# Performance work log

Hardware: AMD Instinct MI355X
Metric: run time of the kernel (lower is better)

The kernel has to match this reference:

```python
import jax, jax.numpy as jnp
import numpy as np

N, E, F_IN, HID, HEADS, C, NCLS, NG, NCONV = 50000, 800000, 128, 128, 8, 16, 10, 64, 3
EPS = 1e-5
NEG_SLOPE = 0.2


def bn_eval(x, p):
    # p: [4, dim] = (gamma, beta, running_mean, running_var); eval-mode BatchNorm1d
    g, b, m, v = p[0], p[1], p[2], p[3]
    return g * (x - m) * jax.lax.rsqrt(v + EPS) + b


def gat_conv(x, src, dst, W, a_src, a_dst, bias):
    # PyG GATConv, concat=True, add_self_loops=True, eval (no dropout)
    h = (x @ W).reshape(N, HEADS, C)                    # [N,H,C]
    alpha_s = jnp.sum(h * a_src[None], axis=-1)         # [N,H]
    alpha_d = jnp.sum(h * a_dst[None], axis=-1)         # [N,H]
    loop = jnp.arange(N)
    s = jnp.concatenate([src, loop])                    # [E+N]
    d = jnp.concatenate([dst, loop])
    logits = jax.nn.leaky_relu(alpha_s[s] + alpha_d[d], NEG_SLOPE)   # [E+N,H]
    mx = jax.lax.stop_gradient(jax.ops.segment_max(logits, d, num_segments=N))
    ex = jnp.exp(logits - mx[d])
    denom = jax.ops.segment_sum(ex, d, num_segments=N)
    alpha = ex / (denom[d] + 1e-16)                     # segment softmax over dst
    msg = h[s] * alpha[:, :, None]                      # [E+N,H,C]
    out = jax.ops.segment_sum(msg, d, num_segments=N)   # [N,H,C]
    return out.reshape(N, HEADS * C) + bias


def setup_inputs() -> dict:
    key = jax.random.key(0)
    ks = jax.random.split(key, 16)

    def bn_p(dim):
        return jnp.stack([jnp.ones(dim), jnp.full((dim,), 1e-4), jnp.zeros(dim), jnp.ones(dim)])

    sc = 0.05
    inp = {
        "x": jax.random.normal(ks[0], (N, F_IN), jnp.float32),
        "edge_index": jax.random.randint(ks[1], (2, E), 0, N),
        "batch": jnp.sort(jax.random.randint(ks[2], (N,), 0, NG)),
        "bn_feat_params": bn_p(F_IN),
        "w_feat": jax.random.normal(ks[3], (F_IN, HID), jnp.float32) * sc,
        "b_feat": jnp.zeros((HID,), jnp.float32),
        "bns_conv_params": jnp.stack([bn_p(HID)] * NCONV),
        "gat_w": jax.random.normal(ks[4], (NCONV, HID, HID), jnp.float32) * sc,
        "gat_att_src": jax.random.normal(ks[5], (NCONV, HEADS, C), jnp.float32) * sc,
        "gat_att_dst": jax.random.normal(ks[6], (NCONV, HEADS, C), jnp.float32) * sc,
        "gat_b": jnp.zeros((NCONV, HID), jnp.float32),
        "bns_fc_params": jnp.stack([bn_p(HID)] * 1),
        "fc_w": jax.random.normal(ks[7], (1, HID, HID), jnp.float32) * sc,
        "fc_b": jnp.zeros((1, HID), jnp.float32),
        "bn_hidden_params": bn_p(HID),
        "w_class": jax.random.normal(ks[8], (HID, NCLS), jnp.float32) * sc,
        "b_class": jnp.zeros((NCLS,), jnp.float32),
    }
    return inp


def reference(x, edge_index, batch, bn_feat_params, w_feat, b_feat, bns_conv_params,
              gat_w, gat_att_src, gat_att_dst, gat_b, bns_fc_params, fc_w, fc_b,
              bn_hidden_params, w_class, b_class):
    src, dst = edge_index[0], edge_index[1]
    h = bn_eval(x, bn_feat_params)
    h = jax.nn.relu(h @ w_feat + b_feat)             # GCNConv(gfn=True) == linear
    for i in range(NCONV):
        h = bn_eval(h, bns_conv_params[i])
        h = jax.nn.relu(gat_conv(h, src, dst, gat_w[i], gat_att_src[i], gat_att_dst[i], gat_b[i]))
    g = jax.ops.segment_sum(h, batch, num_segments=NG)   # global_add_pool -> [NG,HID]
    for i in range(fc_w.shape[0]):
        g = jax.nn.relu(bn_eval(g, bns_fc_params[i]) @ fc_w[i] + fc_b[i])
    g = bn_eval(g, bn_hidden_params)
    logits = g @ w_class + b_class
    return jax.nn.log_softmax(logits, axis=-1)
```

## Files before the change

### kernel.cpp

```cpp
#include <hip/hip_runtime.h>

#define NN 50000
#define E_EDGES 800000
#define F_INN 128
#define HIDD 128
#define HEADS 8
#define CDIM 16
#define NCLS 10
#define NGG 64
#define NCONV 3
#define EPSS 1e-5f
#define NEG_SLOPE 0.2f

#define WROWS 144
#define WSTRIDE (WROWS * 128)
#define BSTRIDE 144

#define BSH 7
#define BSZ 128
#define NB ((NN + BSZ - 1) / BSZ)
#define STAGE_CAP 16
#define BIN_BLOCKS 256
#define BIN_CHUNK (E_EDGES / BIN_BLOCKS)
#define SORT_BUF 4608
#define BUCKET_PAD 896
#define PW_KCH 32
#define GTILES ((NN + 127) / 128)

typedef __attribute__((ext_vector_type(8))) short short8;
typedef __attribute__((ext_vector_type(4))) float f32x4;

__device__ __forceinline__ float lrelu(float x) { return x > 0.f ? x : NEG_SLOPE * x; }

__device__ __forceinline__ float bf2f(ushort u) {
    union { unsigned int i; float f; } v;
    v.i = ((unsigned int)u) << 16;
    return v.f;
}
__device__ __forceinline__ float bflo(unsigned int x) {
    union { unsigned int i; float f; } v; v.i = x << 16; return v.f;
}
__device__ __forceinline__ float bfhi(unsigned int x) {
    union { unsigned int i; float f; } v; v.i = x & 0xffff0000u; return v.f;
}
__device__ __forceinline__ ushort f2bf(float f) {
    union { float f; unsigned int i; } v;
    v.f = f;
    unsigned int r = (v.i + 0x7fffu + ((v.i >> 16) & 1u)) >> 16;
    return (ushort)r;
}
__device__ __forceinline__ unsigned char f2fp8(float f) {
    int r = __builtin_amdgcn_cvt_pk_fp8_f32(f, f, 0, false);
    return (unsigned char)(r & 0xff);
}

__global__ __launch_bounds__(256) void prep_all(
    const float* __restrict__ bn_feat, const float* __restrict__ w_feat,
    const float* __restrict__ b_feat, const float* __restrict__ bns_conv,
    const float* __restrict__ gat_w, const float* __restrict__ att_src,
    const float* __restrict__ att_dst, ushort* __restrict__ Wt,
    float* __restrict__ bp, int* __restrict__ bcnt)
{
    __shared__ __align__(16) char smem[18560];
    int blk = blockIdx.x;
    int t = threadIdx.x;

    if (blk < 16) {
        float* Wl = (float*)smem;
        float* aak = Wl + PW_KCH * 129;
        int layer = blk >> 2;
        int k0 = (blk & 3) * PW_KCH;
        const float* bn; const float* W;
        if (layer == 0) { bn = bn_feat; W = w_feat; }
        else { bn = bns_conv + (layer - 1) * 4 * HIDD; W = gat_w + (size_t)(layer - 1) * HIDD * HIDD; }
        if (t < PW_KCH) {
            int k = k0 + t;
            aak[t] = bn[k] * rsqrtf(bn[3 * HIDD + k] + EPSS);
        }
        for (int i = t; i < PW_KCH * 128; i += 256) {
            int kk = i >> 7, n = i & 127;
            Wl[kk * 129 + n] = W[(size_t)(k0 + kk) * 128 + n];
        }
        __syncthreads();
        ushort* wrow = Wt + (size_t)layer * WSTRIDE;
        for (int i = t; i < 128 * PW_KCH; i += 256) {
            int n = i >> 5, kk = i & 31;
            wrow[n * 128 + k0 + kk] = f2bf(aak[kk] * Wl[kk * 129 + n]);
        }
    } else if (blk < 20) {
        float* ccs = (float*)smem;
        int layer = blk - 16;
        const float* bn; const float* W;
        if (layer == 0) { bn = bn_feat; W = w_feat; }
        else { bn = bns_conv + (layer - 1) * 4 * HIDD; W = gat_w + (size_t)(layer - 1) * HIDD * HIDD; }
        if (t < 128) {
            float a = bn[t] * rsqrtf(bn[3 * HIDD + t] + EPSS);
            ccs[t] = bn[HIDD + t] - bn[2 * HIDD + t] * a;
        }
        __syncthreads();
        if (t < 128) {
            float bacc = (layer == 0) ? b_feat[t] : 0.f;
            for (int k = 0; k < 128; ++k) bacc += ccs[k] * W[(size_t)k * 128 + t];
            bp[layer * BSTRIDE + t] = bacc;
        }
    } else if (blk < 23) {
        float* Wl   = (float*)smem;
        float* redS = (float*)(smem + 16512);
        float* redD = redS + 256;
        int li = blk - 20;
        int L = li + 1;
        const float* bn = bns_conv + li * 4 * HIDD;
        const float* W  = gat_w + (size_t)li * HIDD * HIDD;
        const float* as = att_src + li * HEADS * CDIM;
        const float* ad = att_dst + li * HEADS * CDIM;
        ushort* Wo = Wt + (size_t)L * WSTRIDE;
        int kl = t >> 3, h = t & 7;
        float acc_s = 0.f, acc_d = 0.f;
        for (int c0 = 0; c0 < 4; ++c0) {
            int k0 = c0 * 32;
            __syncthreads();
            for (int i = t; i < 32 * 128; i += 256) {
                int kk = i >> 7, n = i & 127;
                Wl[kk * 129 + n] = W[(size_t)(k0 + kk) * 128 + n];
            }
            __syncthreads();
            int k = k0 + kl;
            float a  = bn[k] * rsqrtf(bn[3 * HIDD + k] + EPSS);
            float cc = bn[HIDD + k] - bn[2 * HIDD + k] * a;
            float ps = 0.f, pd = 0.f;
            #pragma unroll
            for (int c = 0; c < 16; ++c) {
                float wv = Wl[kl * 129 + h * 16 + c];
                ps += wv * as[h * 16 + c];
                pd += wv * ad[h * 16 + c];
            }
            Wo[(128 + h) * 128 + k] = f2bf(a * ps);
            Wo[(136 + h) * 128 + k] = f2bf(a * pd);
            acc_s += cc * ps;
            acc_d += cc * pd;
        }
        redS[t] = acc_s; redD[t] = acc_d;
        __syncthreads();
        if (t < 8) {
            float s = 0.f, d = 0.f;
            for (int q = 0; q < 32; ++q) { s += redS[q * 8 + t]; d += redD[q * 8 + t]; }
            bp[L * BSTRIDE + 128 + t] = s;
            bp[L * BSTRIDE + 136 + t] = d;
        }
    } else {
        for (int i = t; i < NB; i += 256) bcnt[i] = 0;
    }
}

__global__ __launch_bounds__(256) void bucket_hist(const int* __restrict__ dst,
    int* __restrict__ bcnt)
{
    __shared__ int h[NB];
    for (int i = threadIdx.x; i < NB; i += 256) h[i] = 0;
    __syncthreads();
    for (int e = blockIdx.x * 256 + threadIdx.x; e < E_EDGES; e += gridDim.x * 256)
        atomicAdd(&h[dst[e] >> BSH], 1);
    __syncthreads();
    for (int i = threadIdx.x; i < NB; i += 256)
        if (h[i]) atomicAdd(&bcnt[i], h[i]);
}

__global__ __launch_bounds__(512) void bucket_scan(const int* __restrict__ bcnt,
    int* __restrict__ bbase_pad, int* __restrict__ bpos, int* __restrict__ bout)
{
    __shared__ int s2[512], s3[512];
    int t = threadIdx.x;
    int c = (t < NB) ? bcnt[t] : 0;
    int p = (c + 15) & ~15;
    int q = (c + BUCKET_PAD + 7) & ~7;
    s2[t] = p; s3[t] = q;
    __syncthreads();
    for (int d = 1; d < 512; d <<= 1) {
        int a2 = (t >= d) ? s2[t - d] : 0;
        int a3 = (t >= d) ? s3[t - d] : 0;
        __syncthreads();
        s2[t] += a2; s3[t] += a3;
        __syncthreads();
    }
    if (t < NB) {
        int b2 = s2[t] - p;
        bbase_pad[t] = b2;
        bpos[t] = b2;
        bout[t] = s3[t] - q;
    }
}

__global__ __launch_bounds__(256) void bin_edges(const int* __restrict__ src,
    const int* __restrict__ dst, int* __restrict__ bpos, unsigned int* __restrict__ tmp)
{
    __shared__ unsigned int stage[NB * STAGE_CAP];
    __shared__ int scnt[NB];
    int t = threadIdx.x;
    for (int i = t; i < NB; i += 256) scnt[i] = 0;
    __syncthreads();
    int cbeg = blockIdx.x * BIN_CHUNK;
    int cend = cbeg + BIN_CHUNK;
    for (int tb = cbeg; tb < cend; tb += 256) {
        int e = tb + t;
        if (e < cend) {
            int d = dst[e];
            int b = d >> BSH;
            unsigned int pk = ((unsigned int)(d & (BSZ - 1)) << 16) | (unsigned int)src[e];
            int slot = atomicAdd(&scnt[b], 1);
            if (slot < STAGE_CAP) stage[b * STAGE_CAP + slot] = pk;
            else { int g = atomicAdd(&bpos[b], 1); tmp[g] = pk; }
        }
        __syncthreads();
        for (int b = t; b < NB; b += 256) {
            if (scnt[b] >= STAGE_CAP) {
                int g = atomicAdd(&bpos[b], STAGE_CAP);
                #pragma unroll
                for (int j = 0; j < STAGE_CAP; ++j) tmp[g + j] = stage[b * STAGE_CAP + j];
                scnt[b] = 0;
            }
        }
        __syncthreads();
    }
    for (int b = t; b < NB; b += 256) {
        int n = scnt[b];
        if (n > 0) {
            int g = atomicAdd(&bpos[b], n);
            for (int j = 0; j < n; ++j) tmp[g + j] = stage[b * STAGE_CAP + j];
        }
    }
}

__global__ __launch_bounds__(256) void bucket_sort(const int* __restrict__ bcnt,
    const int* __restrict__ bbase_pad, const int* __restrict__ bout,
    const unsigned int* __restrict__ tmp, ushort* __restrict__ csr,
    unsigned int* __restrict__ rowptr)
{
    __shared__ unsigned int buf[SORT_BUF];
    __shared__ int hist[BSZ];
    __shared__ int pex[BSZ];
    __shared__ int cur[BSZ];
    int b = blockIdx.x, t = threadIdx.x;
    int m = bcnt[b];
    if (m > SORT_BUF) m = SORT_BUF;
    int base_in = bbase_pad[b], base_out = bout[b];
    if (t < BSZ) hist[t] = 0;
    __syncthreads();
    for (int i = t; i < m; i += 256) {
        unsigned int pk = tmp[base_in + i];
        buf[i] = pk;
        atomicAdd(&hist[pk >> 16], 1);
    }
    __syncthreads();
    int pd = 0;
    if (t < BSZ) { pd = (hist[t] + 7) & ~7; pex[t] = pd; }
    __syncthreads();
    for (int d = 1; d < BSZ; d <<= 1) {
        int a = (t < BSZ && t >= d) ? pex[t - d] : 0;
        __syncthreads();
        if (t < BSZ) pex[t] += a;
        __syncthreads();
    }
    if (t < BSZ) {
        int ex = pex[t] - pd;
        pex[t] = ex;
        cur[t] = ex;
        int node = b * BSZ + t;
        if (node < NN)
            rowptr[node] = (unsigned int)(base_out + ex) | ((unsigned int)hist[t] << 21);
    }
    __syncthreads();
    for (int i = t; i < m; i += 256) {
        unsigned int pk = buf[i];
        int dl = pk >> 16;
        int p = atomicAdd(&cur[dl], 1);
        csr[base_out + p] = (ushort)(pk & 0xffffu);
    }
    __syncthreads();
    if (t < BSZ) {
        int ex = pex[t], hn = hist[t], pdn = (hn + 7) & ~7;
        for (int i = hn; i < pdn; ++i) csr[base_out + ex + i] = 0;
    }
}

template <int F32IN, int ALPHAS>
__global__ __launch_bounds__(256) void gemm_mfma(const void* __restrict__ Ain,
    const ushort* __restrict__ Wt, const float* __restrict__ bias,
    ushort* __restrict__ Out, unsigned char* __restrict__ h8,
    float* __restrict__ alph_s, float* __restrict__ alph_d, int n, int dorelu)
{
    const int NT = ALPHAS ? 9 : 8;
    int t = threadIdx.x;
    int wave = t >> 6, lane = t & 63;
    int m16 = lane & 15, quad = lane >> 4;
    int rbase = blockIdx.x * 128 + wave * 32;

    short8 afrag[2][4];
    #pragma unroll
    for (int tt = 0; tt < 2; ++tt) {
        int arow_i = rbase + tt * 16 + m16;
        size_t arow = (size_t)(arow_i < n ? arow_i : 0) * HIDD + quad * 8;
        if (F32IN) {
            const float* ap = (const float*)Ain + arow;
            #pragma unroll
            for (int kk = 0; kk < 4; ++kk) {
                float4 lo = *(const float4*)(ap + kk * 32);
                float4 hi = *(const float4*)(ap + kk * 32 + 4);
                short8 f;
                f[0] = (short)f2bf(lo.x); f[1] = (short)f2bf(lo.y);
                f[2] = (short)f2bf(lo.z); f[3] = (short)f2bf(lo.w);
                f[4] = (short)f2bf(hi.x); f[5] = (short)f2bf(hi.y);
                f[6] = (short)f2bf(hi.z); f[7] = (short)f2bf(hi.w);
                afrag[tt][kk] = f;
            }
        } else {
            const ushort* ap = (const ushort*)Ain + arow;
            #pragma unroll
            for (int kk = 0; kk < 4; ++kk)
                afrag[tt][kk] = *(const short8*)(ap + kk * 32);
        }
    }

    f32x4 acc[2][9];
    #pragma unroll
    for (int tt = 0; tt < 2; ++tt)
        #pragma unroll
        for (int nt = 0; nt < NT; ++nt) acc[tt][nt] = (f32x4){0.f, 0.f, 0.f, 0.f};

    #pragma unroll
    for (int nt = 0; nt < NT; ++nt) {
        const ushort* brow = Wt + (size_t)(nt * 16 + m16) * HIDD + quad * 8;
        #pragma unroll
        for (int kk = 0; kk < 4; ++kk) {
            short8 bfrag = *(const short8*)(brow + kk * 32);
            acc[0][nt] = __builtin_amdgcn_mfma_f32_16x16x32_bf16(afrag[0][kk], bfrag, acc[0][nt], 0, 0, 0);
            acc[1][nt] = __builtin_amdgcn_mfma_f32_16x16x32_bf16(afrag[1][kk], bfrag, acc[1][nt], 0, 0, 0);
        }
    }

    #pragma unroll
    for (int tt = 0; tt < 2; ++tt) {
        int tb = rbase + tt * 16;
        #pragma unroll
        for (int nt = 0; nt < 8; ++nt) {
            int col = nt * 16 + m16;
            float bv = bias[col];
            #pragma unroll
            for (int r = 0; r < 4; ++r) {
                int orow = tb + quad * 4 + r;
                if (orow < n) {
                    float v = acc[tt][nt][r] + bv;
                    if (dorelu) v = fmaxf(v, 0.f);
                    Out[(size_t)orow * HIDD + col] = f2bf(v);
                    if (ALPHAS) h8[(size_t)orow * HIDD + col] = f2fp8(v);
                }
            }
        }
        if (ALPHAS) {
            float bv = bias[128 + m16];
            #pragma unroll
            for (int r = 0; r < 4; ++r) {
                int orow = tb + quad * 4 + r;
                if (orow < n) {
                    float v = acc[tt][8][r] + bv;
                    if (m16 < 8) alph_s[orow * HEADS + m16] = v;
                    else         alph_d[orow * HEADS + (m16 - 8)] = v;
                }
            }
        }
    }
}

__global__ __launch_bounds__(256) void gat_aggregate(
    const ushort* __restrict__ h, const unsigned char* __restrict__ h8,
    const float* __restrict__ as, const float* __restrict__ ad,
    const unsigned int* __restrict__ rowptr, const ushort* __restrict__ csr,
    const float* __restrict__ bias, ushort* __restrict__ out)
{
    int wid = (blockIdx.x * 256 + threadIdx.x) >> 6;
    int v = __builtin_amdgcn_readfirstlane(wid);
    if (v >= NN) return;
    int lane = threadIdx.x & 63;
    int hd = lane >> 3;
    int slot = lane & 7;
    int gbase = lane & ~7;
    unsigned int rp = rowptr[v];
    int beg = rp & 0x1FFFFF;
    int cnt = rp >> 21;
    float adv = ad[v * HEADS + hd];

    const unsigned int* h32 = (const unsigned int*)h;
    const ushort* h8v = (const ushort*)h8;

    float wself = __expf(lrelu(as[v * HEADS + hd] + adv));
    unsigned int hv = h32[(size_t)v * 64 + lane];
    float denom = wself;
    float acc0 = wself * bflo(hv);
    float acc1 = wself * bfhi(hv);

    int ngro = (cnt + 7) >> 3;
    if (ngro > 0) {
        const uint4* epk = (const uint4*)(csr + beg);
        int u0[8], u1[8];
        float l_own0, l_own1;
        unsigned int x0[8], x1[8];
        {
            uint4 pk = epk[0];
            u0[0] = pk.x & 0xffff; u0[1] = pk.x >> 16;
            u0[2] = pk.y & 0xffff; u0[3] = pk.y >> 16;
            u0[4] = pk.z & 0xffff; u0[5] = pk.z >> 16;
            u0[6] = pk.w & 0xffff; u0[7] = pk.w >> 16;
            unsigned int d = slot < 4 ? (slot < 2 ? pk.x : pk.y)
                                      : (slot < 6 ? pk.z : pk.w);
            int u_own = (slot & 1) ? (int)(d >> 16) : (int)(d & 0xffff);
            l_own0 = as[u_own * HEADS + hd];
            #pragma unroll
            for (int j = 0; j < 8; ++j) x0[j] = h8v[(size_t)u0[j] * 64 + lane];
        }
        for (int g = 0; g < ngro; ++g) {
            bool more = (g + 1 < ngro);
            if (more) {
                uint4 pk = epk[g + 1];
                u1[0] = pk.x & 0xffff; u1[1] = pk.x >> 16;
                u1[2] = pk.y & 0xffff; u1[3] = pk.y >> 16;
                u1[4] = pk.z & 0xffff; u1[5] = pk.z >> 16;
                u1[6] = pk.w & 0xffff; u1[7] = pk.w >> 16;
                unsigned int d = slot < 4 ? (slot < 2 ? pk.x : pk.y)
                                          : (slot < 6 ? pk.z : pk.w);
                int u_own = (slot & 1) ? (int)(d >> 16) : (int)(d & 0xffff);
                l_own1 = as[u_own * HEADS + hd];
                #pragma unroll
                for (int j = 0; j < 8; ++j) x1[j] = h8v[(size_t)u1[j] * 64 + lane];
            }
            float w_own = __expf(lrelu(l_own0 + adv));
            if (g * 8 + slot >= cnt) w_own = 0.f;
            #pragma unroll
            for (int j = 0; j < 8; ++j) {
                float wj = __shfl(w_own, gbase + j, 64);
                denom += wj;
                acc0 += wj * __builtin_amdgcn_cvt_f32_fp8(x0[j], 0);
                acc1 += wj * __builtin_amdgcn_cvt_f32_fp8(x0[j], 1);
            }
            if (more) {
                l_own0 = l_own1;
                #pragma unroll
                for (int j = 0; j < 8; ++j) { u0[j] = u1[j]; x0[j] = x1[j]; }
            }
        }
    }

    float inv = 1.f / (denom + 1e-16f);
    int c = 2 * lane;
    float o0 = fmaxf(acc0 * inv + bias[c], 0.f);
    float o1 = fmaxf(acc1 * inv + bias[c + 1], 0.f);
    ((unsigned int*)out)[(size_t)v * 64 + lane] =
        (unsigned int)f2bf(o0) | ((unsigned int)f2bf(o1) << 16);
}

__global__ __launch_bounds__(256) void pool_head(const ushort* __restrict__ h,
    const int* __restrict__ batch,
    const float* __restrict__ bns_fc, const float* __restrict__ fc_w,
    const float* __restrict__ fc_b, const float* __restrict__ bn_hid,
    const float* __restrict__ w_class, const float* __restrict__ b_class,
    float* __restrict__ out)
{
    __shared__ float sred[256];
    __shared__ float v1[HIDD];
    __shared__ float v2[HIDD];
    __shared__ float lg[NCLS];
    __shared__ float lse;
    __shared__ int bounds[2];
    int gb = blockIdx.x, t = threadIdx.x;

    if (t < 2) {
        int key = gb + t;
        int lo = 0, hi = NN;
        while (lo < hi) {
            int mid = (lo + hi) >> 1;
            if (batch[mid] < key) lo = mid + 1; else hi = mid;
        }
        bounds[t] = lo;
    }
    __syncthreads();
    int beg = bounds[0], end = bounds[1];

    int half = t >> 7, c = t & 127;
    float a0 = 0.f, a1 = 0.f, a2 = 0.f, a3 = 0.f;
    int r = beg + half;
    for (; r + 6 < end; r += 8) {
        a0 += bf2f(h[(size_t)r * HIDD + c]);
        a1 += bf2f(h[(size_t)(r + 2) * HIDD + c]);
        a2 += bf2f(h[(size_t)(r + 4) * HIDD + c]);
        a3 += bf2f(h[(size_t)(r + 6) * HIDD + c]);
    }
    for (; r < end; r += 2) a0 += bf2f(h[(size_t)r * HIDD + c]);
    sred[t] = (a0 + a1) + (a2 + a3);
    __syncthreads();

    if (t < HIDD) {
        float gv = sred[t] + sred[t + 128];
        float gamma = bns_fc[t], beta = bns_fc[HIDD + t];
        float mu = bns_fc[2 * HIDD + t], var = bns_fc[3 * HIDD + t];
        v1[t] = (gv - mu) * gamma * rsqrtf(var + EPSS) + beta;
    }
    __syncthreads();

    if (t < HIDD) {
        float acc = fc_b[t];
        for (int k = 0; k < HIDD; ++k) acc += v1[k] * fc_w[k * HIDD + t];
        acc = fmaxf(acc, 0.f);
        float gamma = bn_hid[t], beta = bn_hid[HIDD + t];
        float mu = bn_hid[2 * HIDD + t], var = bn_hid[3 * HIDD + t];
        v2[t] = (acc - mu) * gamma * rsqrtf(var + EPSS) + beta;
    }
    __syncthreads();

    if (t < NCLS) {
        float acc2 = b_class[t];
        for (int k = 0; k < HIDD; ++k) acc2 += v2[k] * w_class[k * NCLS + t];
        lg[t] = acc2;
    }
    __syncthreads();
    if (t == 0) {
        float mx = lg[0];
        for (int i = 1; i < NCLS; ++i) mx = fmaxf(mx, lg[i]);
        float ss = 0.f;
        for (int i = 0; i < NCLS; ++i) ss += __expf(lg[i] - mx);
        lse = mx + __logf(ss);
    }
    __syncthreads();
    if (t < NCLS) out[gb * NCLS + t] = lg[t] - lse;
}

extern "C" void kernel_launch(void* const* d_in, const int* in_sizes, int n_in,
                              void* d_out, int out_size, void* d_ws, size_t ws_size,
                              hipStream_t stream)
{
    const float* x        = (const float*)d_in[0];
    const int*   edge     = (const int*)d_in[1];
    const int*   batch    = (const int*)d_in[2];
    const float* bn_feat  = (const float*)d_in[3];
    const float* w_feat   = (const float*)d_in[4];
    const float* b_feat   = (const float*)d_in[5];
    const float* bns_conv = (const float*)d_in[6];
    const float* gat_w    = (const float*)d_in[7];
    const float* att_src  = (const float*)d_in[8];
    const float* att_dst  = (const float*)d_in[9];
    const float* gat_b    = (const float*)d_in[10];
    const float* bns_fc   = (const float*)d_in[11];
    const float* fc_w     = (const float*)d_in[12];
    const float* fc_b     = (const float*)d_in[13];
    const float* bn_hid   = (const float*)d_in[14];
    const float* w_class  = (const float*)d_in[15];
    const float* b_class  = (const float*)d_in[16];
    float* out = (float*)d_out;
    (void)in_sizes; (void)n_in; (void)out_size; (void)ws_size;

    char* ws = (char*)d_ws;
    size_t off = 0;
    auto alloc = [&](size_t bytes) {
        void* p = ws + off;
        off = (off + bytes + 255) & ~(size_t)255;
        return p;
    };
    ushort* Wt        = (ushort*)alloc((size_t)4 * WSTRIDE * sizeof(ushort));
    float*  bp        = (float*)alloc(4 * BSTRIDE * sizeof(float));
    ushort* h_a       = (ushort*)alloc((size_t)NN * HIDD * sizeof(ushort));
    ushort* h_b       = (ushort*)alloc((size_t)NN * HIDD * sizeof(ushort));
    unsigned char* h8 = (unsigned char*)alloc((size_t)NN * HIDD);
    float*  alph_s    = (float*)alloc((size_t)NN * HEADS * sizeof(float));
    float*  alph_d    = (float*)alloc((size_t)NN * HEADS * sizeof(float));
    int*    bcnt      = (int*)alloc(NB * sizeof(int));
    int*    bbase_pad = (int*)alloc(NB * sizeof(int));
    int*    bpos      = (int*)alloc(NB * sizeof(int));
    int*    bout      = (int*)alloc(NB * sizeof(int));
    unsigned int* tmp = (unsigned int*)alloc((size_t)(E_EDGES + NB * STAGE_CAP) * sizeof(unsigned int));
    unsigned int* rowptr = (unsigned int*)alloc((size_t)NN * sizeof(unsigned int));
    ushort* csr       = (ushort*)alloc((size_t)(E_EDGES + NB * BUCKET_PAD + 16) * sizeof(ushort));

    const int* src = edge;
    const int* dst = edge + E_EDGES;

    prep_all<<<24, 256, 0, stream>>>(bn_feat, w_feat, b_feat, bns_conv, gat_w,
                                     att_src, att_dst, Wt, bp, bcnt);
    bucket_hist<<<256, 256, 0, stream>>>(dst, bcnt);
    bucket_scan<<<1, 512, 0, stream>>>(bcnt, bbase_pad, bpos, bout);
    bin_edges<<<BIN_BLOCKS, 256, 0, stream>>>(src, dst, bpos, tmp);
    bucket_sort<<<NB, 256, 0, stream>>>(bcnt, bbase_pad, bout, tmp, csr, rowptr);

    gemm_mfma<1, 0><<<GTILES, 256, 0, stream>>>(x, Wt, bp, h_a,
        nullptr, nullptr, nullptr, NN, 1);

    for (int i = 0; i < NCONV; ++i) {
        gemm_mfma<0, 1><<<GTILES, 256, 0, stream>>>(h_a,
            Wt + (size_t)(i + 1) * WSTRIDE, bp + (i + 1) * BSTRIDE, h_b, h8,
            alph_s, alph_d, NN, 0);
        gat_aggregate<<<(NN + 3) / 4, 256, 0, stream>>>(h_b, h8, alph_s, alph_d,
                                                        rowptr, csr, gat_b + i * HIDD, h_a);
    }

    pool_head<<<NGG, 256, 0, stream>>>(h_a, batch, bns_fc, fc_w, fc_b, bn_hid,
                                       w_class, b_class, out);
}
```

Before: 348.3 us.

## Fuse bucket histogram into prep kernel and split aggregation by channel halves

The destination-bucket histogram moves into extra blocks of the prep kernel, and the counter zeroing becomes a memset, which removes one kernel launch. Graph aggregation is split into two launches, each covering 64 of the 128 channels with one channel per lane and byte-wide FP8 gathers. The split aims to shrink each launch's gather footprint per neighbour row. In exchange it repeats the edge-index loads, attention exps and shuffles twice per layer, and the gathers get narrower.

```diff
diff --git a/kernel.cpp b/kernel.cpp
--- a/kernel.cpp
+++ b/kernel.cpp
@@ -37,12 +37,6 @@
     v.i = ((unsigned int)u) << 16;
     return v.f;
 }
-__device__ __forceinline__ float bflo(unsigned int x) {
-    union { unsigned int i; float f; } v; v.i = x << 16; return v.f;
-}
-__device__ __forceinline__ float bfhi(unsigned int x) {
-    union { unsigned int i; float f; } v; v.i = x & 0xffff0000u; return v.f;
-}
 __device__ __forceinline__ ushort f2bf(float f) {
     union { float f; unsigned int i; } v;
     v.f = f;
@@ -58,8 +52,8 @@
     const float* __restrict__ bn_feat, const float* __restrict__ w_feat,
     const float* __restrict__ b_feat, const float* __restrict__ bns_conv,
     const float* __restrict__ gat_w, const float* __restrict__ att_src,
-    const float* __restrict__ att_dst, ushort* __restrict__ Wt,
-    float* __restrict__ bp, int* __restrict__ bcnt)
+    const float* __restrict__ att_dst, const int* __restrict__ dst,
+    ushort* __restrict__ Wt, float* __restrict__ bp, int* __restrict__ bcnt)
 {
     __shared__ __align__(16) char smem[18560];
     int blk = blockIdx.x;
@@ -148,21 +142,16 @@
             bp[L * BSTRIDE + 136 + t] = d;
         }
     } else {
-        for (int i = t; i < NB; i += 256) bcnt[i] = 0;
-    }
-}
-
-__global__ __launch_bounds__(256) void bucket_hist(const int* __restrict__ dst,
-    int* __restrict__ bcnt)
-{
-    __shared__ int h[NB];
-    for (int i = threadIdx.x; i < NB; i += 256) h[i] = 0;
-    __syncthreads();
-    for (int e = blockIdx.x * 256 + threadIdx.x; e < E_EDGES; e += gridDim.x * 256)
-        atomicAdd(&h[dst[e] >> BSH], 1);
-    __syncthreads();
-    for (int i = threadIdx.x; i < NB; i += 256)
-        if (h[i]) atomicAdd(&bcnt[i], h[i]);
+        int* hh = (int*)smem;
+        for (int i = t; i < NB; i += 256) hh[i] = 0;
+        __syncthreads();
+        int cblk = blk - 23;
+        for (int e = cblk * 256 + t; e < E_EDGES; e += 256 * 256)
+            atomicAdd(&hh[dst[e] >> BSH], 1);
+        __syncthreads();
+        for (int i = t; i < NB; i += 256)
+            if (hh[i]) atomicAdd(&bcnt[i], hh[i]);
+    }
 }
 
 __global__ __launch_bounds__(512) void bucket_scan(const int* __restrict__ bcnt,
@@ -374,28 +363,27 @@
     const ushort* __restrict__ h, const unsigned char* __restrict__ h8,
     const float* __restrict__ as, const float* __restrict__ ad,
     const unsigned int* __restrict__ rowptr, const ushort* __restrict__ csr,
-    const float* __restrict__ bias, ushort* __restrict__ out)
+    const float* __restrict__ bias, ushort* __restrict__ out, int ch0)
 {
     int wid = (blockIdx.x * 256 + threadIdx.x) >> 6;
     int v = __builtin_amdgcn_readfirstlane(wid);
     if (v >= NN) return;
     int lane = threadIdx.x & 63;
+    int c = ch0 + lane;
     int hd = lane >> 3;
+    int chd = c >> 4;
     int slot = lane & 7;
-    int gbase = lane & ~7;
     unsigned int rp = rowptr[v];
     int beg = rp & 0x1FFFFF;
     int cnt = rp >> 21;
+
     float adv = ad[v * HEADS + hd];
 
-    const unsigned int* h32 = (const unsigned int*)h;
-    const ushort* h8v = (const ushort*)h8;
-
-    float wself = __expf(lrelu(as[v * HEADS + hd] + adv));
-    unsigned int hv = h32[(size_t)v * 64 + lane];
+    float wself_own = __expf(lrelu(as[v * HEADS + hd] + adv));
+    float wself = __shfl(wself_own, (chd << 3), 64);
+    float selfv = bf2f(h[(size_t)v * HIDD + c]);
     float denom = wself;
-    float acc0 = wself * bflo(hv);
-    float acc1 = wself * bfhi(hv);
+    float acc = wself * selfv;
 
     int ngro = (cnt + 7) >> 3;
     if (ngro > 0) {
@@ -414,7 +402,7 @@
             int u_own = (slot & 1) ? (int)(d >> 16) : (int)(d & 0xffff);
             l_own0 = as[u_own * HEADS + hd];
             #pragma unroll
-            for (int j = 0; j < 8; ++j) x0[j] = h8v[(size_t)u0[j] * 64 + lane];
+            for (int j = 0; j < 8; ++j) x0[j] = h8[(size_t)u0[j] * HIDD + c];
         }
         for (int g = 0; g < ngro; ++g) {
             bool more = (g + 1 < ngro);
@@ -429,16 +417,15 @@
                 int u_own = (slot & 1) ? (int)(d >> 16) : (int)(d & 0xffff);
                 l_own1 = as[u_own * HEADS + hd];
                 #pragma unroll
-                for (int j = 0; j < 8; ++j) x1[j] = h8v[(size_t)u1[j] * 64 + lane];
+                for (int j = 0; j < 8; ++j) x1[j] = h8[(size_t)u1[j] * HIDD + c];
             }
             float w_own = __expf(lrelu(l_own0 + adv));
             if (g * 8 + slot >= cnt) w_own = 0.f;
             #pragma unroll
             for (int j = 0; j < 8; ++j) {
-                float wj = __shfl(w_own, gbase + j, 64);
+                float wj = __shfl(w_own, (chd << 3) + j, 64);
                 denom += wj;
-                acc0 += wj * __builtin_amdgcn_cvt_f32_fp8(x0[j], 0);
-                acc1 += wj * __builtin_amdgcn_cvt_f32_fp8(x0[j], 1);
+                acc += wj * __builtin_amdgcn_cvt_f32_fp8(x0[j], 0);
             }
             if (more) {
                 l_own0 = l_own1;
@@ -449,11 +436,8 @@
     }
 
     float inv = 1.f / (denom + 1e-16f);
-    int c = 2 * lane;
-    float o0 = fmaxf(acc0 * inv + bias[c], 0.f);
-    float o1 = fmaxf(acc1 * inv + bias[c + 1], 0.f);
-    ((unsigned int*)out)[(size_t)v * 64 + lane] =
-        (unsigned int)f2bf(o0) | ((unsigned int)f2bf(o1) << 16);
+    float o = fmaxf(acc * inv + bias[c], 0.f);
+    out[(size_t)v * HIDD + c] = f2bf(o);
 }
 
 __global__ __launch_bounds__(256) void pool_head(const ushort* __restrict__ h,
@@ -580,9 +564,9 @@
     const int* src = edge;
     const int* dst = edge + E_EDGES;
 
-    prep_all<<<24, 256, 0, stream>>>(bn_feat, w_feat, b_feat, bns_conv, gat_w,
-                                     att_src, att_dst, Wt, bp, bcnt);
-    bucket_hist<<<256, 256, 0, stream>>>(dst, bcnt);
+    hipMemsetAsync(bcnt, 0, NB * sizeof(int), stream);
+    prep_all<<<279, 256, 0, stream>>>(bn_feat, w_feat, b_feat, bns_conv, gat_w,
+                                      att_src, att_dst, dst, Wt, bp, bcnt);
     bucket_scan<<<1, 512, 0, stream>>>(bcnt, bbase_pad, bpos, bout);
     bin_edges<<<BIN_BLOCKS, 256, 0, stream>>>(src, dst, bpos, tmp);
     bucket_sort<<<NB, 256, 0, stream>>>(bcnt, bbase_pad, bout, tmp, csr, rowptr);
@@ -595,7 +579,9 @@
             Wt + (size_t)(i + 1) * WSTRIDE, bp + (i + 1) * BSTRIDE, h_b, h8,
             alph_s, alph_d, NN, 0);
         gat_aggregate<<<(NN + 3) / 4, 256, 0, stream>>>(h_b, h8, alph_s, alph_d,
-                                                        rowptr, csr, gat_b + i * HIDD, h_a);
+                                                        rowptr, csr, gat_b + i * HIDD, h_a, 0);
+        gat_aggregate<<<(NN + 3) / 4, 256, 0, stream>>>(h_b, h8, alph_s, alph_d,
+                                                        rowptr, csr, gat_b + i * HIDD, h_a, 64);
     }
 
     pool_head<<<NGG, 256, 0, stream>>>(h_a, batch, bns_fc, fc_w, fc_b, bn_hid,
```

Measured after the change: 408.3 us. 1.17x slower.
